# Performance work log

Measured on AMD Instinct MI355X. Metric: run time of the kernel, lower is better.

Reference implementation:

```python
import jax, jax.numpy as jnp
import numpy as np

B, T, E, H = 2, 1024, 1024, 16
HD = E // H
TEMP = 0.5


def setup_inputs() -> dict:
    key = jax.random.key(0)
    ks = jax.random.split(key, 20)
    d = {
        "query1": jax.random.normal(ks[0], (B, T, E), jnp.float32),
        "query2": jax.random.normal(ks[1], (B, T, E), jnp.float32),
        "key": jax.random.normal(ks[2], (B, T, E), jnp.float32),
        "value": jax.random.normal(ks[3], (B, T, E), jnp.float32),
    }
    s = 1.0 / np.sqrt(E)
    names = ["Wq", "Wq2", "Wq3", "Wk", "Wv", "Wo"]
    for i, n in enumerate(names):
        d[n] = jax.random.normal(ks[4 + i], (E, E), jnp.float32) * s
        d["b" + n[1:]] = jax.random.normal(ks[10 + i], (E,), jnp.float32) * 0.01
    return d


def _heads(x):
    # [B,T,E] -> [B,H,T,HD]
    b, t, _ = x.shape
    return x.reshape(b, t, H, HD).transpose(0, 2, 1, 3)


def reference(query1, query2, key, value,
              Wq, bq, Wq2, bq2, Wq3, bq3, Wk, bk, Wv, bv, Wo, bo):
    q = _heads(query1 @ Wq.T + bq)
    q2 = _heads(query2 @ Wq2.T + bq2)
    q3 = _heads(key @ Wq3.T + bq3)
    k = _heads(key @ Wk.T + bk)
    v = _heads(value @ Wv.T + bv)
    b, _, t, _ = q.shape
    scale = 1.0 / np.sqrt(HD)

    def global_attn(qx):
        s = jnp.einsum('bhtd,bhsd->bhts', qx, k) * scale  # [B,H,T,T]
        # global softmax over flattened T*T, temperature-scaled, times T
        a = jax.nn.softmax((s / TEMP).reshape(b, H, t * t), axis=-1)
        return a.reshape(b, H, t, t) * t

    a1 = global_attn(q)
    a2 = global_attn(q2)
    a3 = global_attn(q3)
    attn_out = jnp.einsum('bhts,bhsd->bthd', (a1 + a2 + a3) / 3.0, v)
    attn_out = attn_out.reshape(b, t, E)
    output = attn_out @ Wo.T + bo
    return output, a1
```

## Files before the change

### kernel.cpp

```cpp
#include <hip/hip_runtime.h>
#include <hip/hip_bf16.h>


#define B_ 2
#define T_ 1024
#define E_ 1024
#define H_ 16
#define HD_ 64
#define BH_ 32

typedef float f32x4 __attribute__((ext_vector_type(4)));
typedef short bfrag __attribute__((ext_vector_type(8)));

__device__ __forceinline__ unsigned short f2b(float f) {
  unsigned int u = __float_as_uint(f);
  u += 0x7fffu + ((u >> 16) & 1u);
  return (unsigned short)(u >> 16);
}

struct CvtArgs { const float* src[10]; unsigned short* dst[10]; int n[10]; };

__global__ __launch_bounds__(256) void cvt_kernel(CvtArgs a) {
  const int z = blockIdx.y;
  const float* __restrict__ s = a.src[z];
  unsigned short* __restrict__ d = a.dst[z];
  const int n = a.n[z];
  const int stride = gridDim.x * 256 * 4;
  for (int i = (blockIdx.x * 256 + threadIdx.x) * 4; i < n; i += stride) {
    float4 v = *(const float4*)(s + i);
    ushort4 o;
    o.x = f2b(v.x); o.y = f2b(v.y); o.z = f2b(v.z); o.w = f2b(v.w);
    *(ushort4*)(d + i) = o;
  }
}

__device__ __forceinline__ void mm128_core(const unsigned short* __restrict__ A,
                                           const unsigned short* __restrict__ W,
                                           int m0, int n0,
                                           unsigned short* As, unsigned short* Bs,
                                           f32x4 acc[4][4]) {
  const int tid  = threadIdx.x;
  const int lane = tid & 63, w = tid >> 6;
  const int lrow = lane & 15, quad = lane >> 4;
  const int wm = (w >> 1) * 64, wn = (w & 1) * 64;
  const int srow = tid >> 2, soff = (tid & 3) * 8;

  const unsigned short* Ar0 = A + (size_t)(m0 + srow) * E_ + soff;
  const unsigned short* Ar1 = Ar0 + (size_t)64 * E_;
  const unsigned short* Br0 = W + (size_t)(n0 + srow) * E_ + soff;
  const unsigned short* Br1 = Br0 + (size_t)64 * E_;

  for (int k0 = 0; k0 < E_; k0 += 32) {
    int4 a0 = *(const int4*)(Ar0 + k0);
    int4 a1 = *(const int4*)(Ar1 + k0);
    int4 b0 = *(const int4*)(Br0 + k0);
    int4 b1 = *(const int4*)(Br1 + k0);
    __syncthreads();
    *(int4*)(As + srow * 32 + soff)        = a0;
    *(int4*)(As + (srow + 64) * 32 + soff) = a1;
    *(int4*)(Bs + srow * 32 + soff)        = b0;
    *(int4*)(Bs + (srow + 64) * 32 + soff) = b1;
    __syncthreads();
    bfrag af[4], bf_[4];
#pragma unroll
    for (int mt = 0; mt < 4; mt++)
      af[mt] = *(const bfrag*)(As + (wm + mt * 16 + lrow) * 32 + quad * 8);
#pragma unroll
    for (int nt = 0; nt < 4; nt++)
      bf_[nt] = *(const bfrag*)(Bs + (wn + nt * 16 + lrow) * 32 + quad * 8);
#pragma unroll
    for (int mt = 0; mt < 4; mt++)
#pragma unroll
      for (int nt = 0; nt < 4; nt++)
        acc[mt][nt] = __builtin_amdgcn_mfma_f32_16x16x32_bf16(af[mt], bf_[nt], acc[mt][nt], 0, 0, 0);
  }
}

struct ProjArgs {
  const unsigned short* X[5];
  const unsigned short* W[5];
  const float* bias[5];
  unsigned short* dst[5];
};

__global__ __launch_bounds__(256) void proj_kernel(ProjArgs pa) {
  __shared__ unsigned short As[128 * 32];
  __shared__ unsigned short Bs[128 * 32];
  const int z = blockIdx.z;
  const int m0 = blockIdx.y * 128, n0 = blockIdx.x * 128;
  f32x4 acc[4][4];
#pragma unroll
  for (int mt = 0; mt < 4; mt++)
#pragma unroll
    for (int nt = 0; nt < 4; nt++) acc[mt][nt] = (f32x4)0.f;

  mm128_core(pa.X[z], pa.W[z], m0, n0, As, Bs, acc);

  const int tid = threadIdx.x, lane = tid & 63, w = tid >> 6;
  const int lrow = lane & 15, quad = lane >> 4;
  const int wm = (w >> 1) * 64, wn = (w & 1) * 64;
  const float* __restrict__ bias = pa.bias[z];
  unsigned short* __restrict__ dst = pa.dst[z];
  float bv[4];
#pragma unroll
  for (int nt = 0; nt < 4; nt++) bv[nt] = bias[n0 + wn + nt * 16 + lrow];
#pragma unroll
  for (int mt = 0; mt < 4; mt++)
#pragma unroll
    for (int nt = 0; nt < 4; nt++)
#pragma unroll
      for (int ii = 0; ii < 4; ii++) {
        const int m = m0 + wm + mt * 16 + quad * 4 + ii;
        const int n = n0 + wn + nt * 16 + lrow;
        const float v = acc[mt][nt][ii] + bv[nt];
        const int b = m >> 10, t = m & 1023, h = n >> 6, dd = n & 63;
        size_t idx;
        if (z == 4)
          idx = ((size_t)((b * H_ + h) * HD_ + dd)) * T_ + t;
        else
          idx = ((size_t)((b * H_ + h) * T_ + t)) * HD_ + dd;
        dst[idx] = f2b(v);
      }
}

__global__ __launch_bounds__(256) void attn_sums_kernel(
    const unsigned short* __restrict__ Q1, const unsigned short* __restrict__ Q2,
    const unsigned short* __restrict__ Q3, const unsigned short* __restrict__ Kh,
    float* __restrict__ sums) {
  const int tid = threadIdx.x, lane = tid & 63, w = tid >> 6;
  const int lrow = lane & 15, quad = lane >> 4;
  const int tw = w >> 1, sw = w & 1;
  const int bh = blockIdx.y;
  const int tb = blockIdx.x * 128 + tw * 64;
  const size_t base = (size_t)bh * T_ * HD_;
  const unsigned short* Qs[3] = {Q1 + base, Q2 + base, Q3 + base};
  const unsigned short* Kb = Kh + base;

  float lsum[3] = {0.f, 0.f, 0.f};
  for (int s0 = 0; s0 < T_; s0 += 128) {
    const int sb = s0 + sw * 64;
#pragma unroll
    for (int i = 0; i < 3; i++) {
      f32x4 acc[4][4];
#pragma unroll
      for (int mt = 0; mt < 4; mt++)
#pragma unroll
        for (int nt = 0; nt < 4; nt++) acc[mt][nt] = (f32x4)0.f;
#pragma unroll
      for (int kk = 0; kk < 2; kk++) {
        bfrag af[4], bf_[4];
#pragma unroll
        for (int mt = 0; mt < 4; mt++)
          af[mt] = *(const bfrag*)(Qs[i] + (size_t)(tb + mt * 16 + lrow) * HD_ + kk * 32 + quad * 8);
#pragma unroll
        for (int nt = 0; nt < 4; nt++)
          bf_[nt] = *(const bfrag*)(Kb + (size_t)(sb + nt * 16 + lrow) * HD_ + kk * 32 + quad * 8);
#pragma unroll
        for (int mt = 0; mt < 4; mt++)
#pragma unroll
          for (int nt = 0; nt < 4; nt++)
            acc[mt][nt] = __builtin_amdgcn_mfma_f32_16x16x32_bf16(af[mt], bf_[nt], acc[mt][nt], 0, 0, 0);
      }
      float s = 0.f;
#pragma unroll
      for (int mt = 0; mt < 4; mt++)
#pragma unroll
        for (int nt = 0; nt < 4; nt++)
#pragma unroll
          for (int ii = 0; ii < 4; ii++)
            s += __expf(acc[mt][nt][ii] * 0.25f);
      lsum[i] += s;
    }
  }
#pragma unroll
  for (int i = 0; i < 3; i++) {
    float v = lsum[i];
    for (int off = 32; off > 0; off >>= 1) v += __shfl_down(v, off, 64);
    if (lane == 0) atomicAdd(&sums[i * BH_ + bh], v);
  }
}

__global__ __launch_bounds__(256) void attn_main_kernel(
    const unsigned short* __restrict__ Q1, const unsigned short* __restrict__ Q2,
    const unsigned short* __restrict__ Q3, const unsigned short* __restrict__ Kh,
    const unsigned short* __restrict__ Vt, const float* __restrict__ sums,
    float* __restrict__ a1out, unsigned short* __restrict__ attn_out) {
  __shared__ unsigned short P[128 * 136];
  const int tid = threadIdx.x, lane = tid & 63, w = tid >> 6;
  const int lrow = lane & 15, quad = lane >> 4;
  const int tw = w >> 1, sw = w & 1, dw = sw;
  const int bh = blockIdx.y;
  const int b = bh >> 4, h = bh & 15;
  const int tb = blockIdx.x * 128 + tw * 64;
  const size_t base = (size_t)bh * T_ * HD_;
  const unsigned short* Qs[3] = {Q1 + base, Q2 + base, Q3 + base};
  const unsigned short* Kb = Kh + base;
  const unsigned short* Vb = Vt + (size_t)bh * HD_ * T_;

  float r[3];
#pragma unroll
  for (int i = 0; i < 3; i++) r[i] = (float)T_ / (3.f * sums[i * BH_ + bh]);
  const float a1s = 3.f * r[0];

  f32x4 oacc[4][2];
#pragma unroll
  for (int mt = 0; mt < 4; mt++) { oacc[mt][0] = (f32x4)0.f; oacc[mt][1] = (f32x4)0.f; }

  for (int s0 = 0; s0 < T_; s0 += 128) {
    const int sb = s0 + sw * 64;
    f32x4 pc[4][4];
#pragma unroll
    for (int mt = 0; mt < 4; mt++)
#pragma unroll
      for (int nt = 0; nt < 4; nt++) pc[mt][nt] = (f32x4)0.f;

#pragma unroll
    for (int i = 0; i < 3; i++) {
      f32x4 acc[4][4];
#pragma unroll
      for (int mt = 0; mt < 4; mt++)
#pragma unroll
        for (int nt = 0; nt < 4; nt++) acc[mt][nt] = (f32x4)0.f;
#pragma unroll
      for (int kk = 0; kk < 2; kk++) {
        bfrag af[4], bf_[4];
#pragma unroll
        for (int mt = 0; mt < 4; mt++)
          af[mt] = *(const bfrag*)(Qs[i] + (size_t)(tb + mt * 16 + lrow) * HD_ + kk * 32 + quad * 8);
#pragma unroll
        for (int nt = 0; nt < 4; nt++)
          bf_[nt] = *(const bfrag*)(Kb + (size_t)(sb + nt * 16 + lrow) * HD_ + kk * 32 + quad * 8);
#pragma unroll
        for (int mt = 0; mt < 4; mt++)
#pragma unroll
          for (int nt = 0; nt < 4; nt++)
            acc[mt][nt] = __builtin_amdgcn_mfma_f32_16x16x32_bf16(af[mt], bf_[nt], acc[mt][nt], 0, 0, 0);
      }
      const float ri = r[i];
#pragma unroll
      for (int mt = 0; mt < 4; mt++)
#pragma unroll
        for (int nt = 0; nt < 4; nt++)
#pragma unroll
          for (int ii = 0; ii < 4; ii++) {
            const float e = __expf(acc[mt][nt][ii] * 0.25f);
            pc[mt][nt][ii] += ri * e;
            if (i == 0) {
              const int t = tb + mt * 16 + quad * 4 + ii;
              const int s = sb + nt * 16 + lrow;
              a1out[((size_t)bh * T_ + t) * T_ + s] = e * a1s;
            }
          }
    }
    __syncthreads();
#pragma unroll
    for (int mt = 0; mt < 4; mt++)
#pragma unroll
      for (int nt = 0; nt < 4; nt++)
#pragma unroll
        for (int ii = 0; ii < 4; ii++) {
          const int tl = tw * 64 + mt * 16 + quad * 4 + ii;
          const int sl = sw * 64 + nt * 16 + lrow;
          P[tl * 136 + sl] = f2b(pc[mt][nt][ii]);
        }
    __syncthreads();
#pragma unroll
    for (int kk = 0; kk < 4; kk++) {
      bfrag pf[4], vf[2];
#pragma unroll
      for (int mt = 0; mt < 4; mt++)
        pf[mt] = *(const bfrag*)(P + (tw * 64 + mt * 16 + lrow) * 136 + kk * 32 + quad * 8);
#pragma unroll
      for (int nt = 0; nt < 2; nt++)
        vf[nt] = *(const bfrag*)(Vb + (size_t)(dw * 32 + nt * 16 + lrow) * T_ + s0 + kk * 32 + quad * 8);
#pragma unroll
      for (int mt = 0; mt < 4; mt++)
#pragma unroll
        for (int nt = 0; nt < 2; nt++)
          oacc[mt][nt] = __builtin_amdgcn_mfma_f32_16x16x32_bf16(pf[mt], vf[nt], oacc[mt][nt], 0, 0, 0);
    }
  }
#pragma unroll
  for (int mt = 0; mt < 4; mt++)
#pragma unroll
    for (int nt = 0; nt < 2; nt++)
#pragma unroll
      for (int ii = 0; ii < 4; ii++) {
        const int t = tb + mt * 16 + quad * 4 + ii;
        const int dd = dw * 32 + nt * 16 + lrow;
        attn_out[((size_t)(b * T_ + t)) * E_ + h * HD_ + dd] = f2b(oacc[mt][nt][ii]);
      }
}

__global__ __launch_bounds__(256) void outproj_kernel(
    const unsigned short* __restrict__ Ab, const unsigned short* __restrict__ Wb,
    const float* __restrict__ bias, float* __restrict__ out) {
  __shared__ unsigned short As[128 * 32];
  __shared__ unsigned short Bs[128 * 32];
  const int m0 = blockIdx.y * 128, n0 = blockIdx.x * 128;
  f32x4 acc[4][4];
#pragma unroll
  for (int mt = 0; mt < 4; mt++)
#pragma unroll
    for (int nt = 0; nt < 4; nt++) acc[mt][nt] = (f32x4)0.f;

  mm128_core(Ab, Wb, m0, n0, As, Bs, acc);

  const int tid = threadIdx.x, lane = tid & 63, w = tid >> 6;
  const int lrow = lane & 15, quad = lane >> 4;
  const int wm = (w >> 1) * 64, wn = (w & 1) * 64;
  float bv[4];
#pragma unroll
  for (int nt = 0; nt < 4; nt++) bv[nt] = bias[n0 + wn + nt * 16 + lrow];
#pragma unroll
  for (int mt = 0; mt < 4; mt++)
#pragma unroll
    for (int nt = 0; nt < 4; nt++)
#pragma unroll
      for (int ii = 0; ii < 4; ii++) {
        const int m = m0 + wm + mt * 16 + quad * 4 + ii;
        const int n = n0 + wn + nt * 16 + lrow;
        out[(size_t)m * E_ + n] = acc[mt][nt][ii] + bv[nt];
      }
}

extern "C" void kernel_launch(void* const* d_in, const int* in_sizes, int n_in,
                              void* d_out, int out_size, void* d_ws, size_t ws_size,
                              hipStream_t stream) {
  const float* q1f  = (const float*)d_in[0];
  const float* q2f  = (const float*)d_in[1];
  const float* keyf = (const float*)d_in[2];
  const float* valf = (const float*)d_in[3];
  const float* Wq  = (const float*)d_in[4];  const float* bq  = (const float*)d_in[5];
  const float* Wq2 = (const float*)d_in[6];  const float* bq2 = (const float*)d_in[7];
  const float* Wq3 = (const float*)d_in[8];  const float* bq3 = (const float*)d_in[9];
  const float* Wk  = (const float*)d_in[10]; const float* bk  = (const float*)d_in[11];
  const float* Wv  = (const float*)d_in[12]; const float* bv  = (const float*)d_in[13];
  const float* Wo  = (const float*)d_in[14]; const float* bo  = (const float*)d_in[15];

  char* ws = (char*)d_ws;
  const size_t MB = 1024 * 1024;
  unsigned short* xq1  = (unsigned short*)(ws + 0 * MB);
  unsigned short* xq2  = (unsigned short*)(ws + 4 * MB);
  unsigned short* xkey = (unsigned short*)(ws + 8 * MB);
  unsigned short* xval = (unsigned short*)(ws + 12 * MB);
  unsigned short* wq   = (unsigned short*)(ws + 16 * MB);
  unsigned short* wq2  = (unsigned short*)(ws + 18 * MB);
  unsigned short* wq3  = (unsigned short*)(ws + 20 * MB);
  unsigned short* wk   = (unsigned short*)(ws + 22 * MB);
  unsigned short* wv   = (unsigned short*)(ws + 24 * MB);
  unsigned short* wo   = (unsigned short*)(ws + 26 * MB);
  unsigned short* Qh1  = (unsigned short*)(ws + 28 * MB);
  unsigned short* Qh2  = (unsigned short*)(ws + 32 * MB);
  unsigned short* Qh3  = (unsigned short*)(ws + 36 * MB);
  unsigned short* Kh   = (unsigned short*)(ws + 40 * MB);
  unsigned short* Vt   = (unsigned short*)(ws + 44 * MB);
  unsigned short* attn = (unsigned short*)(ws + 48 * MB);
  float* sums          = (float*)(ws + 52 * MB);

  CvtArgs ca;
  const float* srcs[10] = {q1f, q2f, keyf, valf, Wq, Wq2, Wq3, Wk, Wv, Wo};
  unsigned short* dsts[10] = {xq1, xq2, xkey, xval, wq, wq2, wq3, wk, wv, wo};
  for (int i = 0; i < 10; i++) { ca.src[i] = srcs[i]; ca.dst[i] = dsts[i]; ca.n[i] = (i < 4) ? 2097152 : 1048576; }
  cvt_kernel<<<dim3(2048, 10), 256, 0, stream>>>(ca);

  hipMemsetAsync(sums, 0, 3 * BH_ * sizeof(float), stream);

  ProjArgs pa;
  const unsigned short* Xs[5] = {xq1, xq2, xkey, xkey, xval};
  const unsigned short* Ws_[5] = {wq, wq2, wq3, wk, wv};
  const float* Bi[5] = {bq, bq2, bq3, bk, bv};
  unsigned short* Ds[5] = {Qh1, Qh2, Qh3, Kh, Vt};
  for (int i = 0; i < 5; i++) { pa.X[i] = Xs[i]; pa.W[i] = Ws_[i]; pa.bias[i] = Bi[i]; pa.dst[i] = Ds[i]; }
  proj_kernel<<<dim3(8, 16, 5), 256, 0, stream>>>(pa);

  attn_sums_kernel<<<dim3(8, BH_), 256, 0, stream>>>(Qh1, Qh2, Qh3, Kh, sums);

  float* out = (float*)d_out;
  attn_main_kernel<<<dim3(8, BH_), 256, 0, stream>>>(Qh1, Qh2, Qh3, Kh, Vt, sums,
                                                     out + 2097152, attn);

  outproj_kernel<<<dim3(8, 16), 256, 0, stream>>>(attn, wo, bo, out);
}
```

Measured before the change: 368.3 us.

## Split attention over key segments, use direct-to-LDS GEMM loads with BK=64

Result: slower. 491.6 us (+33.5%).

```diff
diff --git a/kernel.cpp b/kernel.cpp
--- a/kernel.cpp
+++ b/kernel.cpp
@@ -16,6 +16,12 @@
   unsigned int u = __float_as_uint(f);
   u += 0x7fffu + ((u >> 16) & 1u);
   return (unsigned short)(u >> 16);
+}
+
+__device__ __forceinline__ void gl_lds16(const unsigned short* g, unsigned short* l) {
+  __builtin_amdgcn_global_load_lds(
+      (const __attribute__((address_space(1))) unsigned int*)g,
+      (__attribute__((address_space(3))) unsigned int*)l, 16, 0, 0);
 }
 
 struct CvtArgs { const float* src[10]; unsigned short* dst[10]; int n[10]; };
@@ -34,7 +40,7 @@
   }
 }
 
-__device__ __forceinline__ void mm128_core(const unsigned short* __restrict__ A,
+__device__ __forceinline__ void mm128_bk64(const unsigned short* __restrict__ A,
                                            const unsigned short* __restrict__ W,
                                            int m0, int n0,
                                            unsigned short* As, unsigned short* Bs,
@@ -43,36 +49,41 @@
   const int lane = tid & 63, w = tid >> 6;
   const int lrow = lane & 15, quad = lane >> 4;
   const int wm = (w >> 1) * 64, wn = (w & 1) * 64;
-  const int srow = tid >> 2, soff = (tid & 3) * 8;
-
-  const unsigned short* Ar0 = A + (size_t)(m0 + srow) * E_ + soff;
-  const unsigned short* Ar1 = Ar0 + (size_t)64 * E_;
-  const unsigned short* Br0 = W + (size_t)(n0 + srow) * E_ + soff;
-  const unsigned short* Br1 = Br0 + (size_t)64 * E_;
-
-  for (int k0 = 0; k0 < E_; k0 += 32) {
-    int4 a0 = *(const int4*)(Ar0 + k0);
-    int4 a1 = *(const int4*)(Ar1 + k0);
-    int4 b0 = *(const int4*)(Br0 + k0);
-    int4 b1 = *(const int4*)(Br1 + k0);
+  const int srow = lane >> 3;
+  const int gcol = ((lane & 7) ^ srow) * 8;
+
+  const unsigned short* gA = A + (size_t)(m0 + w * 32 + srow) * E_ + gcol;
+  const unsigned short* gB = W + (size_t)(n0 + w * 32 + srow) * E_ + gcol;
+  unsigned short* lA = As + (w * 32) * 64;
+  unsigned short* lB = Bs + (w * 32) * 64;
+
+  for (int k0 = 0; k0 < E_; k0 += 64) {
     __syncthreads();
-    *(int4*)(As + srow * 32 + soff)        = a0;
-    *(int4*)(As + (srow + 64) * 32 + soff) = a1;
-    *(int4*)(Bs + srow * 32 + soff)        = b0;
-    *(int4*)(Bs + (srow + 64) * 32 + soff) = b1;
+#pragma unroll
+    for (int q = 0; q < 4; q++) {
+      gl_lds16(gA + (size_t)q * 8 * E_ + k0, lA + q * 8 * 64);
+      gl_lds16(gB + (size_t)q * 8 * E_ + k0, lB + q * 8 * 64);
+    }
     __syncthreads();
-    bfrag af[4], bf_[4];
-#pragma unroll
-    for (int mt = 0; mt < 4; mt++)
-      af[mt] = *(const bfrag*)(As + (wm + mt * 16 + lrow) * 32 + quad * 8);
-#pragma unroll
-    for (int nt = 0; nt < 4; nt++)
-      bf_[nt] = *(const bfrag*)(Bs + (wn + nt * 16 + lrow) * 32 + quad * 8);
-#pragma unroll
-    for (int mt = 0; mt < 4; mt++)
-#pragma unroll
-      for (int nt = 0; nt < 4; nt++)
-        acc[mt][nt] = __builtin_amdgcn_mfma_f32_16x16x32_bf16(af[mt], bf_[nt], acc[mt][nt], 0, 0, 0);
+#pragma unroll
+    for (int kk = 0; kk < 2; kk++) {
+      bfrag af[4], bf_[4];
+#pragma unroll
+      for (int mt = 0; mt < 4; mt++) {
+        const int r = wm + mt * 16 + lrow;
+        af[mt] = *(const bfrag*)(As + r * 64 + (((kk * 4 + quad) ^ (r & 7)) * 8));
+      }
+#pragma unroll
+      for (int nt = 0; nt < 4; nt++) {
+        const int r = wn + nt * 16 + lrow;
+        bf_[nt] = *(const bfrag*)(Bs + r * 64 + (((kk * 4 + quad) ^ (r & 7)) * 8));
+      }
+#pragma unroll
+      for (int mt = 0; mt < 4; mt++)
+#pragma unroll
+        for (int nt = 0; nt < 4; nt++)
+          acc[mt][nt] = __builtin_amdgcn_mfma_f32_16x16x32_bf16(af[mt], bf_[nt], acc[mt][nt], 0, 0, 0);
+    }
   }
 }
 
@@ -84,8 +95,8 @@
 };
 
 __global__ __launch_bounds__(256) void proj_kernel(ProjArgs pa) {
-  __shared__ unsigned short As[128 * 32];
-  __shared__ unsigned short Bs[128 * 32];
+  __shared__ unsigned short As[128 * 64];
+  __shared__ unsigned short Bs[128 * 64];
   const int z = blockIdx.z;
   const int m0 = blockIdx.y * 128, n0 = blockIdx.x * 128;
   f32x4 acc[4][4];
@@ -94,7 +105,7 @@
 #pragma unroll
     for (int nt = 0; nt < 4; nt++) acc[mt][nt] = (f32x4)0.f;
 
-  mm128_core(pa.X[z], pa.W[z], m0, n0, As, Bs, acc);
+  mm128_bk64(pa.X[z], pa.W[z], m0, n0, As, Bs, acc);
 
   const int tid = threadIdx.x, lane = tid & 63, w = tid >> 6;
   const int lrow = lane & 15, quad = lane >> 4;
@@ -130,47 +141,49 @@
   const int tid = threadIdx.x, lane = tid & 63, w = tid >> 6;
   const int lrow = lane & 15, quad = lane >> 4;
   const int tw = w >> 1, sw = w & 1;
-  const int bh = blockIdx.y;
+  const int bh = blockIdx.z;
   const int tb = blockIdx.x * 128 + tw * 64;
+  const int sb = blockIdx.y * 128 + sw * 64;
   const size_t base = (size_t)bh * T_ * HD_;
   const unsigned short* Qs[3] = {Q1 + base, Q2 + base, Q3 + base};
   const unsigned short* Kb = Kh + base;
 
-  float lsum[3] = {0.f, 0.f, 0.f};
-  for (int s0 = 0; s0 < T_; s0 += 128) {
-    const int sb = s0 + sw * 64;
-#pragma unroll
-    for (int i = 0; i < 3; i++) {
-      f32x4 acc[4][4];
+  bfrag bf_[2][4];
+#pragma unroll
+  for (int kk = 0; kk < 2; kk++)
+#pragma unroll
+    for (int nt = 0; nt < 4; nt++)
+      bf_[kk][nt] = *(const bfrag*)(Kb + (size_t)(sb + nt * 16 + lrow) * HD_ + kk * 32 + quad * 8);
+
+  float lsum[3];
+#pragma unroll
+  for (int i = 0; i < 3; i++) {
+    f32x4 acc[4][4];
+#pragma unroll
+    for (int mt = 0; mt < 4; mt++)
+#pragma unroll
+      for (int nt = 0; nt < 4; nt++) acc[mt][nt] = (f32x4)0.f;
+#pragma unroll
+    for (int kk = 0; kk < 2; kk++) {
+      bfrag af[4];
 #pragma unroll
       for (int mt = 0; mt < 4; mt++)
-#pragma unroll
-        for (int nt = 0; nt < 4; nt++) acc[mt][nt] = (f32x4)0.f;
-#pragma unroll
-      for (int kk = 0; kk < 2; kk++) {
-        bfrag af[4], bf_[4];
-#pragma unroll
-        for (int mt = 0; mt < 4; mt++)
-          af[mt] = *(const bfrag*)(Qs[i] + (size_t)(tb + mt * 16 + lrow) * HD_ + kk * 32 + quad * 8);
+        af[mt] = *(const bfrag*)(Qs[i] + (size_t)(tb + mt * 16 + lrow) * HD_ + kk * 32 + quad * 8);
+#pragma unroll
+      for (int mt = 0; mt < 4; mt++)
 #pragma unroll
         for (int nt = 0; nt < 4; nt++)
-          bf_[nt] = *(const bfrag*)(Kb + (size_t)(sb + nt * 16 + lrow) * HD_ + kk * 32 + quad * 8);
-#pragma unroll
-        for (int mt = 0; mt < 4; mt++)
-#pragma unroll
-          for (int nt = 0; nt < 4; nt++)
-            acc[mt][nt] = __builtin_amdgcn_mfma_f32_16x16x32_bf16(af[mt], bf_[nt], acc[mt][nt], 0, 0, 0);
-      }
-      float s = 0.f;
-#pragma unroll
-      for (int mt = 0; mt < 4; mt++)
-#pragma unroll
-        for (int nt = 0; nt < 4; nt++)
-#pragma unroll
-          for (int ii = 0; ii < 4; ii++)
-            s += __expf(acc[mt][nt][ii] * 0.25f);
-      lsum[i] += s;
+          acc[mt][nt] = __builtin_amdgcn_mfma_f32_16x16x32_bf16(af[mt], bf_[kk][nt], acc[mt][nt], 0, 0, 0);
     }
+    float s = 0.f;
+#pragma unroll
+    for (int mt = 0; mt < 4; mt++)
+#pragma unroll
+      for (int nt = 0; nt < 4; nt++)
+#pragma unroll
+        for (int ii = 0; ii < 4; ii++)
+          s += __expf(acc[mt][nt][ii] * 0.25f);
+    lsum[i] = s;
   }
 #pragma unroll
   for (int i = 0; i < 3; i++) {
@@ -184,13 +197,13 @@
     const unsigned short* __restrict__ Q1, const unsigned short* __restrict__ Q2,
     const unsigned short* __restrict__ Q3, const unsigned short* __restrict__ Kh,
     const unsigned short* __restrict__ Vt, const float* __restrict__ sums,
-    float* __restrict__ a1out, unsigned short* __restrict__ attn_out) {
+    float* __restrict__ a1out, float* __restrict__ Opart) {
   __shared__ unsigned short P[128 * 136];
   const int tid = threadIdx.x, lane = tid & 63, w = tid >> 6;
   const int lrow = lane & 15, quad = lane >> 4;
   const int tw = w >> 1, sw = w & 1, dw = sw;
-  const int bh = blockIdx.y;
-  const int b = bh >> 4, h = bh & 15;
+  const int bh = blockIdx.z;
+  const int seg = blockIdx.y;
   const int tb = blockIdx.x * 128 + tw * 64;
   const size_t base = (size_t)bh * T_ * HD_;
   const unsigned short* Qs[3] = {Q1 + base, Q2 + base, Q3 + base};
@@ -206,14 +219,9 @@
 #pragma unroll
   for (int mt = 0; mt < 4; mt++) { oacc[mt][0] = (f32x4)0.f; oacc[mt][1] = (f32x4)0.f; }
 
-  for (int s0 = 0; s0 < T_; s0 += 128) {
+  for (int s0i = 0; s0i < 2; s0i++) {
+    const int s0 = seg * 256 + s0i * 128;
     const int sb = s0 + sw * 64;
-    f32x4 pc[4][4];
-#pragma unroll
-    for (int mt = 0; mt < 4; mt++)
-#pragma unroll
-      for (int nt = 0; nt < 4; nt++) pc[mt][nt] = (f32x4)0.f;
-
 #pragma unroll
     for (int i = 0; i < 3; i++) {
       f32x4 acc[4][4];
@@ -237,6 +245,7 @@
             acc[mt][nt] = __builtin_amdgcn_mfma_f32_16x16x32_bf16(af[mt], bf_[nt], acc[mt][nt], 0, 0, 0);
       }
       const float ri = r[i];
+      __syncthreads();
 #pragma unroll
       for (int mt = 0; mt < 4; mt++)
 #pragma unroll
@@ -244,42 +253,33 @@
 #pragma unroll
           for (int ii = 0; ii < 4; ii++) {
             const float e = __expf(acc[mt][nt][ii] * 0.25f);
-            pc[mt][nt][ii] += ri * e;
+            const int tl = tw * 64 + mt * 16 + quad * 4 + ii;
+            const int sl = sw * 64 + nt * 16 + lrow;
+            P[tl * 136 + sl] = f2b(ri * e);
             if (i == 0) {
-              const int t = tb + mt * 16 + quad * 4 + ii;
-              const int s = sb + nt * 16 + lrow;
-              a1out[((size_t)bh * T_ + t) * T_ + s] = e * a1s;
+              const int t = blockIdx.x * 128 + tl;
+              a1out[((size_t)bh * T_ + t) * T_ + s0 + sl] = e * a1s;
             }
           }
-    }
-    __syncthreads();
-#pragma unroll
-    for (int mt = 0; mt < 4; mt++)
-#pragma unroll
-      for (int nt = 0; nt < 4; nt++)
-#pragma unroll
-        for (int ii = 0; ii < 4; ii++) {
-          const int tl = tw * 64 + mt * 16 + quad * 4 + ii;
-          const int sl = sw * 64 + nt * 16 + lrow;
-          P[tl * 136 + sl] = f2b(pc[mt][nt][ii]);
-        }
-    __syncthreads();
-#pragma unroll
-    for (int kk = 0; kk < 4; kk++) {
-      bfrag pf[4], vf[2];
-#pragma unroll
-      for (int mt = 0; mt < 4; mt++)
-        pf[mt] = *(const bfrag*)(P + (tw * 64 + mt * 16 + lrow) * 136 + kk * 32 + quad * 8);
-#pragma unroll
-      for (int nt = 0; nt < 2; nt++)
-        vf[nt] = *(const bfrag*)(Vb + (size_t)(dw * 32 + nt * 16 + lrow) * T_ + s0 + kk * 32 + quad * 8);
-#pragma unroll
-      for (int mt = 0; mt < 4; mt++)
+      __syncthreads();
+#pragma unroll
+      for (int kk = 0; kk < 4; kk++) {
+        bfrag pf[4], vf[2];
+#pragma unroll
+        for (int mt = 0; mt < 4; mt++)
+          pf[mt] = *(const bfrag*)(P + (tw * 64 + mt * 16 + lrow) * 136 + kk * 32 + quad * 8);
 #pragma unroll
         for (int nt = 0; nt < 2; nt++)
-          oacc[mt][nt] = __builtin_amdgcn_mfma_f32_16x16x32_bf16(pf[mt], vf[nt], oacc[mt][nt], 0, 0, 0);
+          vf[nt] = *(const bfrag*)(Vb + (size_t)(dw * 32 + nt * 16 + lrow) * T_ + s0 + kk * 32 + quad * 8);
+#pragma unroll
+        for (int mt = 0; mt < 4; mt++)
+#pragma unroll
+          for (int nt = 0; nt < 2; nt++)
+            oacc[mt][nt] = __builtin_amdgcn_mfma_f32_16x16x32_bf16(pf[mt], vf[nt], oacc[mt][nt], 0, 0, 0);
+      }
     }
   }
+  float* Ob = Opart + (size_t)seg * 2097152 + (size_t)bh * 65536;
 #pragma unroll
   for (int mt = 0; mt < 4; mt++)
 #pragma unroll
@@ -288,15 +288,35 @@
       for (int ii = 0; ii < 4; ii++) {
         const int t = tb + mt * 16 + quad * 4 + ii;
         const int dd = dw * 32 + nt * 16 + lrow;
-        attn_out[((size_t)(b * T_ + t)) * E_ + h * HD_ + dd] = f2b(oacc[mt][nt][ii]);
-      }
+        Ob[(size_t)t * 64 + dd] = oacc[mt][nt][ii];
+      }
+}
+
+__global__ __launch_bounds__(256) void reduce_kernel(const float* __restrict__ Op,
+                                                     unsigned short* __restrict__ attn) {
+  const int flat = blockIdx.x * 256 + threadIdx.x;
+  const int dq = (flat & 15) * 4;
+  const int t  = (flat >> 4) & 1023;
+  const int bh = flat >> 14;
+  const int b = bh >> 4, h = bh & 15;
+  const size_t poff = (size_t)bh * 65536 + (size_t)t * 64 + dq;
+  float4 s0 = *(const float4*)(Op + poff);
+  float4 s1 = *(const float4*)(Op + 2097152 + poff);
+  float4 s2 = *(const float4*)(Op + 2 * 2097152 + poff);
+  float4 s3 = *(const float4*)(Op + 3 * (size_t)2097152 + poff);
+  ushort4 o;
+  o.x = f2b(s0.x + s1.x + s2.x + s3.x);
+  o.y = f2b(s0.y + s1.y + s2.y + s3.y);
+  o.z = f2b(s0.z + s1.z + s2.z + s3.z);
+  o.w = f2b(s0.w + s1.w + s2.w + s3.w);
+  *(ushort4*)(attn + ((size_t)(b * T_ + t)) * E_ + h * HD_ + dq) = o;
 }
 
 __global__ __launch_bounds__(256) void outproj_kernel(
     const unsigned short* __restrict__ Ab, const unsigned short* __restrict__ Wb,
     const float* __restrict__ bias, float* __restrict__ out) {
-  __shared__ unsigned short As[128 * 32];
-  __shared__ unsigned short Bs[128 * 32];
+  __shared__ unsigned short As[128 * 64];
+  __shared__ unsigned short Bs[128 * 64];
   const int m0 = blockIdx.y * 128, n0 = blockIdx.x * 128;
   f32x4 acc[4][4];
 #pragma unroll
@@ -304,7 +324,7 @@
 #pragma unroll
     for (int nt = 0; nt < 4; nt++) acc[mt][nt] = (f32x4)0.f;
 
-  mm128_core(Ab, Wb, m0, n0, As, Bs, acc);
+  mm128_bk64(Ab, Wb, m0, n0, As, Bs, acc);
 
   const int tid = threadIdx.x, lane = tid & 63, w = tid >> 6;
   const int lrow = lane & 15, quad = lane >> 4;
@@ -356,7 +376,8 @@
   unsigned short* Kh   = (unsigned short*)(ws + 40 * MB);
   unsigned short* Vt   = (unsigned short*)(ws + 44 * MB);
   unsigned short* attn = (unsigned short*)(ws + 48 * MB);
-  float* sums          = (float*)(ws + 52 * MB);
+  float* Opart         = (float*)(ws + 52 * MB);
+  float* sums          = (float*)(ws + 84 * MB);
 
   CvtArgs ca;
   const float* srcs[10] = {q1f, q2f, keyf, valf, Wq, Wq2, Wq3, Wk, Wv, Wo};
@@ -374,11 +395,13 @@
   for (int i = 0; i < 5; i++) { pa.X[i] = Xs[i]; pa.W[i] = Ws_[i]; pa.bias[i] = Bi[i]; pa.dst[i] = Ds[i]; }
   proj_kernel<<<dim3(8, 16, 5), 256, 0, stream>>>(pa);
 
-  attn_sums_kernel<<<dim3(8, BH_), 256, 0, stream>>>(Qh1, Qh2, Qh3, Kh, sums);
+  attn_sums_kernel<<<dim3(8, 8, BH_), 256, 0, stream>>>(Qh1, Qh2, Qh3, Kh, sums);
 
   float* out = (float*)d_out;
-  attn_main_kernel<<<dim3(8, BH_), 256, 0, stream>>>(Qh1, Qh2, Qh3, Kh, Vt, sums,
-                                                     out + 2097152, attn);
+  attn_main_kernel<<<dim3(8, 4, BH_), 256, 0, stream>>>(Qh1, Qh2, Qh3, Kh, Vt, sums,
+                                                        out + 2097152, Opart);
+
+  reduce_kernel<<<dim3(2048), 256, 0, stream>>>(Opart, attn);
 
   outproj_kernel<<<dim3(8, 16), 256, 0, stream>>>(attn, wo, bo, out);
 }
```
